# Kernel tuning notes

Hardware: AMD Instinct MI355X
Metric: run time of the kernel (lower is better)

Reference implementation:

```python
import jax, jax.numpy as jnp
import numpy as np

D_MODEL = 1024
NUM_HEADS = 16
NUM_KV_HEADS = 4
D_K = D_MODEL // NUM_HEADS  # 64
GROUP = NUM_HEADS // NUM_KV_HEADS  # 4
ROPE_BASE = 10000.0
NEG = -10000.0


def _rope_cos_sin(seq_len, d_k, dtype):
    # matches standard RotaryEmbedding: inv_freq over even dims, emb = cat(freqs, freqs)
    inv_freq = 1.0 / (ROPE_BASE ** (jnp.arange(0, d_k, 2, dtype=jnp.float32) / d_k))
    t = jnp.arange(seq_len, dtype=jnp.float32)
    freqs = jnp.einsum('s,f->sf', t, inv_freq)          # [S, d_k/2]
    emb = jnp.concatenate([freqs, freqs], axis=-1)       # [S, d_k]
    return jnp.cos(emb).astype(dtype), jnp.sin(emb).astype(dtype)


def _apply_rope(x, cos, sin):
    # x: [B, H, S, d_k]; cos/sin: [S, d_k] broadcast over B, H
    half = x.shape[-1] // 2
    x1, x2 = x[..., :half], x[..., half:]
    rotated = jnp.concatenate([-x2, x1], axis=-1)
    return x * cos + rotated * sin


def setup_inputs() -> dict:
    key = jax.random.key(0)
    ks = jax.random.split(key, 7)
    B, S = 2, 2048
    scale = 1.0 / np.sqrt(D_MODEL)
    return {
        'query': jax.random.normal(ks[0], (B, S, D_MODEL), dtype=jnp.float32),
        'key': jax.random.normal(ks[1], (B, S, D_MODEL), dtype=jnp.float32),
        'value': jax.random.normal(ks[2], (B, S, D_MODEL), dtype=jnp.float32),
        'Wq': jax.random.normal(ks[3], (D_MODEL, D_MODEL), dtype=jnp.float32) * scale,
        'Wk': jax.random.normal(ks[4], (NUM_KV_HEADS * D_K, D_MODEL), dtype=jnp.float32) * scale,
        'Wv': jax.random.normal(ks[5], (NUM_KV_HEADS * D_K, D_MODEL), dtype=jnp.float32) * scale,
        'Wo': jax.random.normal(ks[6], (D_MODEL, D_MODEL), dtype=jnp.float32) * scale,
    }


def reference(query, key, value, Wq, Wk, Wv, Wo):
    B, Sq, _ = query.shape
    Sk = key.shape[1]
    # projections (nn.Linear: x @ W.T)
    Q = (query @ Wq.T).reshape(B, Sq, NUM_HEADS, D_K).transpose(0, 2, 1, 3)      # [B,H,Sq,dk]
    K = (key @ Wk.T).reshape(B, Sk, NUM_KV_HEADS, D_K).transpose(0, 2, 1, 3)      # [B,Hkv,Sk,dk]
    V = (value @ Wv.T).reshape(B, Sk, NUM_KV_HEADS, D_K).transpose(0, 2, 1, 3)    # [B,Hkv,Sk,dk]
    # RoPE
    cos, sin = _rope_cos_sin(Sq, D_K, Q.dtype)
    Q = _apply_rope(Q, cos, sin)
    K = _apply_rope(K, cos[:Sk], sin[:Sk])
    # GQA attention without explicitly materializing expanded K/V:
    # group query heads as [B, Hkv, G, Sq, dk]
    Qg = Q.reshape(B, NUM_KV_HEADS, GROUP, Sq, D_K)
    scores = jnp.einsum('bhgqd,bhkd->bhgqk', Qg, K) / jnp.sqrt(jnp.float32(D_K))  # [B,Hkv,G,Sq,Sk]
    causal = jnp.tril(jnp.ones((Sq, Sk), dtype=bool))
    scores = jnp.where(causal, scores, jnp.float32(NEG))
    probs = jax.nn.softmax(scores, axis=-1)
    out = jnp.einsum('bhgqk,bhkd->bhgqd', probs, V)                                # [B,Hkv,G,Sq,dk]
    out = out.reshape(B, NUM_HEADS, Sq, D_K).transpose(0, 2, 1, 3).reshape(B, Sq, D_MODEL)
    return out @ Wo.T
```

## Files before the change

### kernel.cpp

```cpp
#include <hip/hip_runtime.h>
#include <hip/hip_bf16.h>
#include <stdint.h>

typedef __attribute__((ext_vector_type(4))) float f32x4;
typedef __attribute__((ext_vector_type(8))) short short8;

#define S_LEN 2048
#define BATCH 2
#define NH 16
#define NKV 4
#define DK 64

__device__ __forceinline__ ushort f2bf(float f) {
  __hip_bfloat16 h = __float2bfloat16(f);
  ushort u; __builtin_memcpy(&u, &h, 2); return u;
}
__device__ __forceinline__ float bf2f(ushort h) {
  union { uint32_t u; float f; } v; v.u = ((uint32_t)h) << 16;
  return v.f;
}

__device__ __forceinline__ void gld16(const ushort* g, ushort* l) {
  __builtin_amdgcn_global_load_lds((const __attribute__((address_space(1))) void*)g,
                                   (__attribute__((address_space(3))) void*)l,
                                   16, 0, 0);
}

template<int CTRL>
__device__ __forceinline__ float dpp_movf(float x) {
  return __int_as_float(__builtin_amdgcn_update_dpp(0, __float_as_int(x), CTRL, 0xF, 0xF, true));
}
__device__ __forceinline__ float rowred_sum16(float v) {
  v += dpp_movf<0xB1>(v);
  v += dpp_movf<0x4E>(v);
  v += dpp_movf<0x141>(v);
  v += dpp_movf<0x140>(v);
  return v;
}

__global__ void preproc_kernel(const float* __restrict__ q, const float* __restrict__ k,
                               const float* __restrict__ v, ushort* __restrict__ oq,
                               ushort* __restrict__ ok, ushort* __restrict__ ov,
                               const float* __restrict__ w0, const float* __restrict__ w1,
                               const float* __restrict__ w2, const float* __restrict__ w3,
                               ushort* __restrict__ o0, ushort* __restrict__ o1,
                               ushort* __restrict__ o2, ushort* __restrict__ o3,
                               float* __restrict__ tab) {
  const int id = blockIdx.x, tid = threadIdx.x;
  if (id < 12288) {
    int y = id >> 12;
    int i = ((id & 4095) << 8) + tid;
    const float* in = y == 0 ? q : (y == 1 ? k : v);
    ushort* out = y == 0 ? oq : (y == 1 ? ok : ov);
    float4 x = ((const float4*)in)[i];
    ushort4 o;
    o.x = f2bf(x.x); o.y = f2bf(x.y); o.z = f2bf(x.z); o.w = f2bf(x.w);
    ((ushort4*)out)[i] = o;
  } else if (id < 16384) {
    int wid = id - 12288;
    int y = wid >> 10;
    int n4 = (y == 0 || y == 3) ? 262144 : 65536;
    int i = ((wid & 1023) << 8) + tid;
    if (i >= n4) return;
    const float* in = y == 0 ? w0 : y == 1 ? w1 : y == 2 ? w2 : w3;
    ushort* out = y == 0 ? o0 : y == 1 ? o1 : y == 2 ? o2 : o3;
    float4 x = ((const float4*)in)[i];
    ushort4 o;
    o.x = f2bf(x.x); o.y = f2bf(x.y); o.z = f2bf(x.z); o.w = f2bf(x.w);
    ((ushort4*)out)[i] = o;
  } else {
    int j = ((id - 16384) << 8) + tid;
    int s = j >> 5, f = j & 31;
    float freq = (float)s * powf(10000.0f, -(float)f / 32.0f);
    tab[j] = cosf(freq);
    tab[65536 + j] = sinf(freq);
  }
}

template<int EPI>
__device__ __forceinline__ void gemm_body(const ushort* __restrict__ A,
                                          const ushort* __restrict__ W,
                                          void* __restrict__ Cout,
                                          const float* __restrict__ tab,
                                          int N, int K, int bx, int by,
                                          ushort* Al, ushort* Wl) {
  const int t = threadIdx.x;
  const int lane = t & 63;
  const int w = t >> 6;
  const int wr = w >> 1, wc = w & 1;
  const int m0 = bx * 64, n0 = by * 128;
  const int g = lane >> 4, q16 = lane & 15;

  f32x4 acc[2][4] = {};

  const int lrow = lane >> 2, lcol = (lane & 3) * 8;
  const ushort* Ap  = A + (size_t)(m0 + w * 16 + lrow) * K + lcol;
  const ushort* Wp0 = W + (size_t)(n0 + w * 32 + lrow) * K + lcol;
  const ushort* Wp1 = W + (size_t)(n0 + w * 32 + 16 + lrow) * K + lcol;
  ushort* Ab  = &Al[(w * 16) * 32];
  ushort* Wb0 = &Wl[(w * 32) * 32];
  ushort* Wb1 = &Wl[(w * 32 + 16) * 32];

  const int KSTEPS = K >> 5;
  for (int kt = 0; kt < KSTEPS; ++kt) {
    const int k0 = kt << 5;
    __syncthreads();
    gld16(Ap + k0, Ab);
    gld16(Wp0 + k0, Wb0);
    gld16(Wp1 + k0, Wb1);
    __syncthreads();
    short8 af[2], wf[4];
    #pragma unroll
    for (int i = 0; i < 2; ++i)
      af[i] = *(const short8*)&Al[(wr * 32 + i * 16 + q16) * 32 + g * 8];
    #pragma unroll
    for (int j = 0; j < 4; ++j)
      wf[j] = *(const short8*)&Wl[(wc * 64 + j * 16 + q16) * 32 + g * 8];
    #pragma unroll
    for (int i = 0; i < 2; ++i)
      #pragma unroll
      for (int j = 0; j < 4; ++j)
        acc[i][j] = __builtin_amdgcn_mfma_f32_16x16x32_bf16(af[i], wf[j], acc[i][j], 0, 0, 0);
  }

  if (EPI == 0) {
    #pragma unroll
    for (int i = 0; i < 2; ++i)
      #pragma unroll
      for (int j = 0; j < 4; ++j) {
        int row0 = m0 + wr * 32 + i * 16 + g * 4;
        int col  = n0 + wc * 64 + j * 16 + q16;
        #pragma unroll
        for (int r = 0; r < 4; ++r)
          ((float*)Cout)[(size_t)(row0 + r) * N + col] = acc[i][j][r];
      }
  } else if (EPI == 1 || EPI == 2) {
    const int NHE = (EPI == 1) ? NH : NKV;
    const float qscale = (EPI == 1) ? 0.125f : 1.0f;
    const int h = (n0 + wc * 64) >> 6;
    ushort* O = (ushort*)Cout;
    #pragma unroll
    for (int i = 0; i < 2; ++i)
      #pragma unroll
      for (int j = 0; j < 2; ++j) {
        const int d = j * 16 + q16;
        #pragma unroll
        for (int r = 0; r < 4; ++r) {
          int row = m0 + wr * 32 + i * 16 + g * 4 + r;
          int b = row >> 11, s = row & 2047;
          float x1 = acc[i][j][r], x2 = acc[i][j + 2][r];
          float c = tab[s * 32 + d], sn = tab[65536 + s * 32 + d];
          ushort* base = O + ((size_t)(b * NHE + h) * 2048 + s) * 64;
          base[d]      = f2bf((x1 * c - x2 * sn) * qscale);
          base[d + 32] = f2bf((x2 * c + x1 * sn) * qscale);
        }
      }
  } else {
    const int h = (n0 + wc * 64) >> 6;
    ushort* O = (ushort*)Cout;
    #pragma unroll
    for (int i = 0; i < 2; ++i) {
      int row0 = m0 + wr * 32 + i * 16 + g * 4;
      int b = row0 >> 11, s0 = row0 & 2047;
      #pragma unroll
      for (int j = 0; j < 4; ++j) {
        const int d = j * 16 + q16;
        ushort4 o;
        o.x = f2bf(acc[i][j][0]); o.y = f2bf(acc[i][j][1]);
        o.z = f2bf(acc[i][j][2]); o.w = f2bf(acc[i][j][3]);
        *(ushort4*)(O + ((size_t)(b * NKV + h) * 64 + d) * 2048 + s0) = o;
      }
    }
  }
}

__global__ __launch_bounds__(256) void qkv_gemm_kernel(
    const ushort* __restrict__ qbf, const ushort* __restrict__ wqb, ushort* __restrict__ Qh,
    const ushort* __restrict__ kbf, const ushort* __restrict__ wkb, ushort* __restrict__ Kh,
    const ushort* __restrict__ vbf, const ushort* __restrict__ wvb, ushort* __restrict__ Vt,
    const float* __restrict__ tab) {
  __shared__ ushort Al[64 * 32];
  __shared__ ushort Wl[128 * 32];
  const int id = blockIdx.x;
  if (id < 128) {
    gemm_body<2>(kbf, wkb, Kh, tab, 256, 1024, id & 63, id >> 6, Al, Wl);
  } else if (id < 256) {
    const int i = id - 128;
    gemm_body<3>(vbf, wvb, Vt, tab, 256, 1024, i & 63, i >> 6, Al, Wl);
  } else {
    const int i = id - 256;
    gemm_body<1>(qbf, wqb, Qh, tab, 1024, 1024, i & 63, i >> 6, Al, Wl);
  }
}

__global__ __launch_bounds__(256) void o_gemm_kernel(const ushort* __restrict__ AO,
                                                     const ushort* __restrict__ wob,
                                                     float* __restrict__ out) {
  __shared__ ushort Al[64 * 32];
  __shared__ ushort Wl[128 * 32];
  gemm_body<0>(AO, wob, out, nullptr, 1024, 1024, blockIdx.x & 63, blockIdx.x >> 6, Al, Wl);
}

__global__ __launch_bounds__(256) void fattn_kernel(const ushort* __restrict__ Qh,
                                                    const ushort* __restrict__ Kh,
                                                    const ushort* __restrict__ Vt,
                                                    ushort* __restrict__ AO) {
  __shared__ ushort Klds[2][4096];
  __shared__ ushort Vlds[2][4096];
  __shared__ ushort Plds[4][1024];
  const int t = threadIdx.x, lane = t & 63, wv = t >> 6;
  const int g = lane >> 4, q16 = lane & 15;

  const int hh = blockIdx.y;
  const int b = hh >> 4, h = hh & 15;
  const int kvh = h >> 2;
  const ushort* Kbase = Kh + (size_t)(b * 4 + kvh) * 2048 * 64;
  const ushort* Vbase = Vt + (size_t)(b * 4 + kvh) * 64 * 2048;

  const int r3 = lane >> 3, c3 = lane & 7;
  const int swz = (c3 ^ r3) << 3;
  const int call0 = wv * 2;

  for (int pass = 0; pass < 2; ++pass) {
    const int qt = pass ? (31 - (int)blockIdx.x) : (int)blockIdx.x;
    const int q0 = qt * 64 + wv * 16;
    const ushort* Qbase = Qh + ((size_t)hh * 2048 + q0) * 64;

    short8 aq[2];
    aq[0] = *(const short8*)(Qbase + (size_t)q16 * 64 + g * 8);
    aq[1] = *(const short8*)(Qbase + (size_t)q16 * 64 + 32 + g * 8);

    f32x4 acc[4] = {};
    float lsum[4] = {0.f, 0.f, 0.f, 0.f};

    const int nkb = qt + 1;

    __syncthreads();
    #pragma unroll
    for (int c = 0; c < 2; ++c) {
      int call = call0 + c;
      int row = call * 8 + r3;
      gld16(Kbase + (size_t)row * 64 + swz, &Klds[0][call * 512]);
      gld16(Vbase + (size_t)row * 2048 + swz, &Vlds[0][call * 512]);
    }

    int buf = 0;
    for (int kb = 0; kb < nkb; ++kb) {
      __syncthreads();
      if (kb + 1 < nkb) {
        const int k0n = (kb + 1) * 64;
        #pragma unroll
        for (int c = 0; c < 2; ++c) {
          int call = call0 + c;
          int row = call * 8 + r3;
          gld16(Kbase + (size_t)(k0n + row) * 64 + swz, &Klds[buf ^ 1][call * 512]);
          gld16(Vbase + (size_t)row * 2048 + k0n + swz, &Vlds[buf ^ 1][call * 512]);
        }
      }
      const ushort* Kl = Klds[buf];
      const ushort* Vl = Vlds[buf];
      const int k0 = kb * 64;

      f32x4 sA[4] = {};
      __builtin_amdgcn_s_setprio(1);
      #pragma unroll
      for (int kk = 0; kk < 2; ++kk)
        #pragma unroll
        for (int nt = 0; nt < 4; ++nt) {
          int row = nt * 16 + q16;
          int slot = ((kk << 2) | g) ^ (q16 & 7);
          short8 bk = *(const short8*)(Kl + row * 64 + (slot << 3));
          sA[nt] = __builtin_amdgcn_mfma_f32_16x16x32_bf16(aq[kk], bk, sA[nt], 0, 0, 0);
        }
      __builtin_amdgcn_s_setprio(0);

      if (kb == nkb - 1) {
        #pragma unroll
        for (int nt = 0; nt < 4; ++nt)
          #pragma unroll
          for (int r = 0; r < 4; ++r) {
            int col = k0 + nt * 16 + q16, row = q0 + g * 4 + r;
            if (col > row) sA[nt][r] = -1e30f;
          }
      }

      float ps[4][4];
      #pragma unroll
      for (int nt = 0; nt < 4; ++nt)
        #pragma unroll
        for (int r = 0; r < 4; ++r)
          ps[nt][r] = __expf(sA[nt][r]);
      #pragma unroll
      for (int r = 0; r < 4; ++r)
        lsum[r] += (ps[0][r] + ps[1][r]) + (ps[2][r] + ps[3][r]);

      #pragma unroll
      for (int nt = 0; nt < 4; ++nt)
        #pragma unroll
        for (int r = 0; r < 4; ++r) {
          int pr = g * 4 + r;
          Plds[wv][pr * 64 + ((nt * 16 + q16) ^ ((pr & 7) << 3))] = f2bf(ps[nt][r]);
        }
      __builtin_amdgcn_s_setprio(1);
      #pragma unroll
      for (int kk2 = 0; kk2 < 2; ++kk2) {
        int slot = ((kk2 << 2) | g) ^ (q16 & 7);
        short8 pa = *(const short8*)(&Plds[wv][q16 * 64 + (slot << 3)]);
        #pragma unroll
        for (int dt = 0; dt < 4; ++dt) {
          int rv = dt * 16 + q16;
          short8 bv = *(const short8*)(Vl + rv * 64 + (slot << 3));
          acc[dt] = __builtin_amdgcn_mfma_f32_16x16x32_bf16(pa, bv, acc[dt], 0, 0, 0);
        }
      }
      __builtin_amdgcn_s_setprio(0);

      buf ^= 1;
    }

    float linv[4];
    #pragma unroll
    for (int r = 0; r < 4; ++r) linv[r] = 1.0f / rowred_sum16(lsum[r]);
    #pragma unroll
    for (int dt = 0; dt < 4; ++dt)
      #pragma unroll
      for (int r = 0; r < 4; ++r) {
        float o = acc[dt][r] * linv[r];
        AO[((size_t)(b * 2048) + q0 + g * 4 + r) * 1024 + h * 64 + dt * 16 + q16] = f2bf(o);
      }
  }
}

extern "C" void kernel_launch(void* const* d_in, const int* in_sizes, int n_in,
                              void* d_out, int out_size, void* d_ws, size_t ws_size,
                              hipStream_t stream) {
  const float* query = (const float*)d_in[0];
  const float* key   = (const float*)d_in[1];
  const float* value = (const float*)d_in[2];
  const float* Wq    = (const float*)d_in[3];
  const float* Wk    = (const float*)d_in[4];
  const float* Wv    = (const float*)d_in[5];
  const float* Wo    = (const float*)d_in[6];
  float* out = (float*)d_out;

  char* ws = (char*)d_ws;
  size_t off = 0;
  auto alloc = [&](size_t bytes) {
    void* p = ws + off; off += (bytes + 255) & ~255ULL; return p;
  };
  ushort* qbf = (ushort*)alloc(4096ULL * 1024 * 2);
  ushort* kbf = (ushort*)alloc(4096ULL * 1024 * 2);
  ushort* vbf = (ushort*)alloc(4096ULL * 1024 * 2);
  ushort* wqb = (ushort*)alloc(1024ULL * 1024 * 2);
  ushort* wkb = (ushort*)alloc(256ULL * 1024 * 2);
  ushort* wvb = (ushort*)alloc(256ULL * 1024 * 2);
  ushort* wob = (ushort*)alloc(1024ULL * 1024 * 2);
  ushort* Qh  = (ushort*)alloc(4096ULL * 1024 * 2);
  ushort* Kh  = (ushort*)alloc(4096ULL * 256 * 2);
  ushort* Vt  = (ushort*)alloc(4096ULL * 256 * 2);
  ushort* AO  = (ushort*)alloc(4096ULL * 1024 * 2);
  float*  tab = (float*)alloc(2048ULL * 32 * 4 * 2);

  preproc_kernel<<<16640, 256, 0, stream>>>(query, key, value, qbf, kbf, vbf,
                                            Wq, Wk, Wv, Wo, wqb, wkb, wvb, wob,
                                            (float*)tab);

  qkv_gemm_kernel<<<768, 256, 0, stream>>>(qbf, wqb, Qh, kbf, wkb, Kh, vbf, wvb, Vt, (float*)tab);

  fattn_kernel<<<dim3(16, 32), 256, 0, stream>>>(Qh, Kh, Vt, AO);

  o_gemm_kernel<<<512, 256, 0, stream>>>(AO, wob, out);
}
```

Before: 105.0 us.

## Fuse fp32-to-bf16 activation conversion into QKV GEMM A-tile loads

The separate preprocessing pass that converted query/key/value from fp32 to bf16 is removed. The QKV GEMM now loads fp32 activation tiles straight into LDS with an XOR-swizzled layout and converts them to bf16 while building MFMA fragments. This drops a full read/write round trip over the activations, but doubles the A-tile LDS footprint and global load bytes per K-step. The same tile is also converted again in every N-block that reads it.

New measurement: 98.83 us, median of 2. 1.06x faster.

```diff
diff --git a/kernel.cpp b/kernel.cpp
--- a/kernel.cpp
+++ b/kernel.cpp
@@ -20,7 +20,7 @@
   return v.f;
 }
 
-__device__ __forceinline__ void gld16(const ushort* g, ushort* l) {
+__device__ __forceinline__ void gld16(const void* g, void* l) {
   __builtin_amdgcn_global_load_lds((const __attribute__((address_space(1))) void*)g,
                                    (__attribute__((address_space(3))) void*)l,
                                    16, 0, 0);
@@ -38,29 +38,15 @@
   return v;
 }
 
-__global__ void preproc_kernel(const float* __restrict__ q, const float* __restrict__ k,
-                               const float* __restrict__ v, ushort* __restrict__ oq,
-                               ushort* __restrict__ ok, ushort* __restrict__ ov,
-                               const float* __restrict__ w0, const float* __restrict__ w1,
+__global__ void preproc_kernel(const float* __restrict__ w0, const float* __restrict__ w1,
                                const float* __restrict__ w2, const float* __restrict__ w3,
                                ushort* __restrict__ o0, ushort* __restrict__ o1,
                                ushort* __restrict__ o2, ushort* __restrict__ o3,
                                float* __restrict__ tab) {
-  const int id = blockIdx.x, tid = threadIdx.x;
-  if (id < 12288) {
-    int y = id >> 12;
-    int i = ((id & 4095) << 8) + tid;
-    const float* in = y == 0 ? q : (y == 1 ? k : v);
-    ushort* out = y == 0 ? oq : (y == 1 ? ok : ov);
-    float4 x = ((const float4*)in)[i];
-    ushort4 o;
-    o.x = f2bf(x.x); o.y = f2bf(x.y); o.z = f2bf(x.z); o.w = f2bf(x.w);
-    ((ushort4*)out)[i] = o;
-  } else if (id < 16384) {
-    int wid = id - 12288;
-    int y = wid >> 10;
+  const int y = blockIdx.y, tid = threadIdx.x;
+  if (y < 4) {
     int n4 = (y == 0 || y == 3) ? 262144 : 65536;
-    int i = ((wid & 1023) << 8) + tid;
+    int i = (blockIdx.x << 8) + tid;
     if (i >= n4) return;
     const float* in = y == 0 ? w0 : y == 1 ? w1 : y == 2 ? w2 : w3;
     ushort* out = y == 0 ? o0 : y == 1 ? o1 : y == 2 ? o2 : o3;
@@ -69,7 +55,8 @@
     o.x = f2bf(x.x); o.y = f2bf(x.y); o.z = f2bf(x.z); o.w = f2bf(x.w);
     ((ushort4*)out)[i] = o;
   } else {
-    int j = ((id - 16384) << 8) + tid;
+    int j = (blockIdx.x << 8) + tid;
+    if (j >= 65536) return;
     int s = j >> 5, f = j & 31;
     float freq = (float)s * powf(10000.0f, -(float)f / 32.0f);
     tab[j] = cosf(freq);
@@ -77,13 +64,13 @@
   }
 }
 
-template<int EPI>
-__device__ __forceinline__ void gemm_body(const ushort* __restrict__ A,
+template<int EPI, int AF32>
+__device__ __forceinline__ void gemm_body(const void* __restrict__ Avp,
                                           const ushort* __restrict__ W,
                                           void* __restrict__ Cout,
                                           const float* __restrict__ tab,
                                           int N, int K, int bx, int by,
-                                          ushort* Al, ushort* Wl) {
+                                          void* AlV, ushort* Wl) {
   const int t = threadIdx.x;
   const int lane = t & 63;
   const int w = t >> 6;
@@ -94,25 +81,56 @@
   f32x4 acc[2][4] = {};
 
   const int lrow = lane >> 2, lcol = (lane & 3) * 8;
-  const ushort* Ap  = A + (size_t)(m0 + w * 16 + lrow) * K + lcol;
+  const int r8 = lane >> 3, c8 = lane & 7;
+
   const ushort* Wp0 = W + (size_t)(n0 + w * 32 + lrow) * K + lcol;
   const ushort* Wp1 = W + (size_t)(n0 + w * 32 + 16 + lrow) * K + lcol;
-  ushort* Ab  = &Al[(w * 16) * 32];
   ushort* Wb0 = &Wl[(w * 32) * 32];
   ushort* Wb1 = &Wl[(w * 32 + 16) * 32];
+
+  const ushort* Ab16 = nullptr; const float* Af32 = nullptr;
+  if (AF32) Af32 = (const float*)Avp; else Ab16 = (const ushort*)Avp;
 
   const int KSTEPS = K >> 5;
   for (int kt = 0; kt < KSTEPS; ++kt) {
     const int k0 = kt << 5;
     __syncthreads();
-    gld16(Ap + k0, Ab);
+    if (AF32) {
+      float* Alf = (float*)AlV;
+      #pragma unroll
+      for (int c = 0; c < 2; ++c) {
+        int row = w * 16 + c * 8 + r8;
+        gld16(Af32 + (size_t)(m0 + row) * K + k0 + ((c8 ^ r8) << 2),
+              Alf + (size_t)(w * 16 + c * 8) * 32);
+      }
+    } else {
+      ushort* Alh = (ushort*)AlV;
+      gld16(Ab16 + (size_t)(m0 + w * 16 + lrow) * K + k0 + lcol,
+            Alh + (size_t)(w * 16) * 32);
+    }
     gld16(Wp0 + k0, Wb0);
     gld16(Wp1 + k0, Wb1);
     __syncthreads();
     short8 af[2], wf[4];
     #pragma unroll
-    for (int i = 0; i < 2; ++i)
-      af[i] = *(const short8*)&Al[(wr * 32 + i * 16 + q16) * 32 + g * 8];
+    for (int i = 0; i < 2; ++i) {
+      int row = wr * 32 + i * 16 + q16;
+      if (AF32) {
+        const float* Alf = (const float*)AlV;
+        int s0 = (g * 2) ^ (q16 & 7), s1 = (g * 2 + 1) ^ (q16 & 7);
+        float4 v0 = *(const float4*)&Alf[row * 32 + s0 * 4];
+        float4 v1 = *(const float4*)&Alf[row * 32 + s1 * 4];
+        short8 a;
+        a[0] = (short)f2bf(v0.x); a[1] = (short)f2bf(v0.y);
+        a[2] = (short)f2bf(v0.z); a[3] = (short)f2bf(v0.w);
+        a[4] = (short)f2bf(v1.x); a[5] = (short)f2bf(v1.y);
+        a[6] = (short)f2bf(v1.z); a[7] = (short)f2bf(v1.w);
+        af[i] = a;
+      } else {
+        const ushort* Alh = (const ushort*)AlV;
+        af[i] = *(const short8*)&Alh[row * 32 + g * 8];
+      }
+    }
     #pragma unroll
     for (int j = 0; j < 4; ++j)
       wf[j] = *(const short8*)&Wl[(wc * 64 + j * 16 + q16) * 32 + g * 8];
@@ -175,21 +193,21 @@
 }
 
 __global__ __launch_bounds__(256) void qkv_gemm_kernel(
-    const ushort* __restrict__ qbf, const ushort* __restrict__ wqb, ushort* __restrict__ Qh,
-    const ushort* __restrict__ kbf, const ushort* __restrict__ wkb, ushort* __restrict__ Kh,
-    const ushort* __restrict__ vbf, const ushort* __restrict__ wvb, ushort* __restrict__ Vt,
+    const float* __restrict__ query, const ushort* __restrict__ wqb, ushort* __restrict__ Qh,
+    const float* __restrict__ key,   const ushort* __restrict__ wkb, ushort* __restrict__ Kh,
+    const float* __restrict__ value, const ushort* __restrict__ wvb, ushort* __restrict__ Vt,
     const float* __restrict__ tab) {
-  __shared__ ushort Al[64 * 32];
+  __shared__ float Al[64 * 32];
   __shared__ ushort Wl[128 * 32];
   const int id = blockIdx.x;
   if (id < 128) {
-    gemm_body<2>(kbf, wkb, Kh, tab, 256, 1024, id & 63, id >> 6, Al, Wl);
+    gemm_body<2, 1>(key, wkb, Kh, tab, 256, 1024, id & 63, id >> 6, Al, Wl);
   } else if (id < 256) {
     const int i = id - 128;
-    gemm_body<3>(vbf, wvb, Vt, tab, 256, 1024, i & 63, i >> 6, Al, Wl);
+    gemm_body<3, 1>(value, wvb, Vt, tab, 256, 1024, i & 63, i >> 6, Al, Wl);
   } else {
     const int i = id - 256;
-    gemm_body<1>(qbf, wqb, Qh, tab, 1024, 1024, i & 63, i >> 6, Al, Wl);
+    gemm_body<1, 1>(query, wqb, Qh, tab, 1024, 1024, i & 63, i >> 6, Al, Wl);
   }
 }
 
@@ -198,7 +216,7 @@
                                                      float* __restrict__ out) {
   __shared__ ushort Al[64 * 32];
   __shared__ ushort Wl[128 * 32];
-  gemm_body<0>(AO, wob, out, nullptr, 1024, 1024, blockIdx.x & 63, blockIdx.x >> 6, Al, Wl);
+  gemm_body<0, 0>(AO, wob, out, nullptr, 1024, 1024, blockIdx.x & 63, blockIdx.x >> 6, Al, Wl);
 }
 
 __global__ __launch_bounds__(256) void fattn_kernel(const ushort* __restrict__ Qh,
@@ -348,9 +366,6 @@
   auto alloc = [&](size_t bytes) {
     void* p = ws + off; off += (bytes + 255) & ~255ULL; return p;
   };
-  ushort* qbf = (ushort*)alloc(4096ULL * 1024 * 2);
-  ushort* kbf = (ushort*)alloc(4096ULL * 1024 * 2);
-  ushort* vbf = (ushort*)alloc(4096ULL * 1024 * 2);
   ushort* wqb = (ushort*)alloc(1024ULL * 1024 * 2);
   ushort* wkb = (ushort*)alloc(256ULL * 1024 * 2);
   ushort* wvb = (ushort*)alloc(256ULL * 1024 * 2);
@@ -361,11 +376,11 @@
   ushort* AO  = (ushort*)alloc(4096ULL * 1024 * 2);
   float*  tab = (float*)alloc(2048ULL * 32 * 4 * 2);
 
-  preproc_kernel<<<16640, 256, 0, stream>>>(query, key, value, qbf, kbf, vbf,
-                                            Wq, Wk, Wv, Wo, wqb, wkb, wvb, wob,
-                                            (float*)tab);
-
-  qkv_gemm_kernel<<<768, 256, 0, stream>>>(qbf, wqb, Qh, kbf, wkb, Kh, vbf, wvb, Vt, (float*)tab);
+  preproc_kernel<<<dim3(1024, 5), 256, 0, stream>>>(Wq, Wk, Wv, Wo,
+                                                    wqb, wkb, wvb, wob, (float*)tab);
+
+  qkv_gemm_kernel<<<768, 256, 0, stream>>>(query, wqb, Qh, key, wkb, Kh,
+                                           value, wvb, Vt, (float*)tab);
 
   fattn_kernel<<<dim3(16, 32), 256, 0, stream>>>(Qh, Kh, Vt, AO);
 
```
